# Kernel tuning notes

Measured on AMD Instinct MI355X. Metric: run time of the kernel, lower is better.

## Reference

```python
import jax, jax.numpy as jnp
import numpy as np

NEG_SLOPE = 0.2


def _gat_layer(x, edge_index, W, a_src, a_dst, b):
    """PyG GATConv: linear -> per-edge attention logits -> segment softmax over
    destination -> scatter-add weighted messages. Self-loops added (PyG default)."""
    N = x.shape[0]
    heads, out = a_src.shape
    loops = jnp.arange(N, dtype=edge_index.dtype)
    src = jnp.concatenate([edge_index[0], loops])
    dst = jnp.concatenate([edge_index[1], loops])
    xh = (x @ W).reshape(N, heads, out)                      # [N,H,D]
    alpha_s = (xh * a_src).sum(-1)                           # [N,H]
    alpha_d = (xh * a_dst).sum(-1)                           # [N,H]
    e = jax.nn.leaky_relu(alpha_s[src] + alpha_d[dst], NEG_SLOPE)  # [E,H]
    emax = jax.ops.segment_max(e, dst, num_segments=N)       # [N,H]
    ex = jnp.exp(e - emax[dst])
    den = jax.ops.segment_sum(ex, dst, num_segments=N)
    att = ex / (den[dst] + 1e-16)                            # [E,H]
    msg = xh[src] * att[..., None]                           # [E,H,D]
    o = jax.ops.segment_sum(msg, dst, num_segments=N)        # [N,H,D]
    return o.reshape(N, heads * out) + b


def _single_source_gnn(h, edge_index, params):
    n_layers = len(params)
    for i, (W, a_s, a_d, b) in enumerate(params):
        h = _gat_layer(h, edge_index, W, a_s, a_d, b)
        if i < n_layers - 1:
            h = jax.nn.relu(h)
    return h


def setup_inputs() -> dict:
    key = jax.random.key(0)
    B, N, H, heads, deg = 4, 2000, 64, 4, 32
    E = N * deg
    ks = jax.random.split(key, 20)

    def mk_edge_index(k):
        e = jax.random.randint(k, (2, B, E), 0, N)
        off = (jnp.arange(B) * N)[None, :, None]
        return (e + off).reshape(2, B * E).astype(jnp.int32)

    inp = {
        "h0_flat": jax.random.normal(ks[0], (B * N, H), jnp.float32),
        "edge_index_s1": mk_edge_index(ks[1]),
        "edge_index_s2": mk_edge_index(ks[2]),
    }
    dims = [(H, H * heads), (H * heads, H * heads)]
    i = 3
    for s in ("s1", "s2"):
        for l, (din, dout) in enumerate(dims):
            inp[f"W_{s}_{l}"] = jax.random.normal(ks[i], (din, dout), jnp.float32) * 0.1; i += 1
            inp[f"a_src_{s}_{l}"] = jax.random.normal(ks[i], (heads, H), jnp.float32) * 0.1; i += 1
            inp[f"a_dst_{s}_{l}"] = jax.random.normal(ks[i], (heads, H), jnp.float32) * 0.1; i += 1
            inp[f"b_{s}_{l}"] = jnp.zeros((dout,), jnp.float32)
    inp["batch_size"] = B
    inp["num_stocks"] = N
    return inp


def reference(h0_flat, edge_index_s1, edge_index_s2,
              W_s1_0, a_src_s1_0, a_dst_s1_0, b_s1_0,
              W_s1_1, a_src_s1_1, a_dst_s1_1, b_s1_1,
              W_s2_0, a_src_s2_0, a_dst_s2_0, b_s2_0,
              W_s2_1, a_src_s2_1, a_dst_s2_1, b_s2_1,
              batch_size, num_stocks):
    p1 = [(W_s1_0, a_src_s1_0, a_dst_s1_0, b_s1_0),
          (W_s1_1, a_src_s1_1, a_dst_s1_1, b_s1_1)]
    p2 = [(W_s2_0, a_src_s2_0, a_dst_s2_0, b_s2_0),
          (W_s2_1, a_src_s2_1, a_dst_s2_1, b_s2_1)]
    h1 = _single_source_gnn(h0_flat, edge_index_s1, p1)
    h2 = _single_source_gnn(h0_flat, edge_index_s2, p2)
    # dict of per-source outputs in torch -> stacked [n_sources, B*N, H*heads]
    return jnp.stack([h1, h2])
```

## Files before the change

### kernel.cpp

```cpp
#include <hip/hip_runtime.h>
#include <hip/hip_fp16.h>


#define NEG_SLOPE 0.2f
#define ELLW 96
#define EPT 8
#define NB_PREP 512

typedef _Float16 half8 __attribute__((ext_vector_type(8)));
typedef float floatx4 __attribute__((ext_vector_type(4)));

struct Args {
    const float* h0;
    const int *ei1, *ei2;
    const float *W10, *W11, *W20, *W21;
    const float *as10, *ad10, *b10, *as11, *ad11, *b11;
    const float *as20, *ad20, *b20, *as21, *ad21, *b21;
    _Float16 *Wt10, *Wt20, *Wt11, *Wt21;
    _Float16 *h0h;
    int *cnt, *slots;
    _Float16 *agg1, *agg2;
    _Float16 *xh1, *xh2;
    float *alS1, *alD1, *alS2, *alD2;
    float *out0, *out1;
    int N, E1, E2, AB;
};


__global__ __launch_bounds__(256) void mega_prep_kernel(Args a) {
    int b = blockIdx.x;
    int tid = threadIdx.x;

    if (b < NB_PREP) {
        int flat = b * 256 + tid;
        int GT = NB_PREP * 256;
        int totA = 32768;
        int totB = totA + 131072;
        int totC = totB + a.N * 64;
        for (int i = flat; i < totC; i += GT) {
            if (i < totA) {
                int s = i >> 14, rem = i & 16383;
                int c = rem >> 6, k = rem & 63;
                const float* W = s ? a.W20 : a.W10;
                _Float16* Wt = s ? a.Wt20 : a.Wt10;
                Wt[c * 64 + k] = (_Float16)W[k * 256 + c];
            } else if (i < totB) {
                int i2 = i - totA;
                int s = i2 >> 16, rem = i2 & 65535;
                int c = rem >> 8, k = rem & 255;
                const float* W = s ? a.W21 : a.W11;
                _Float16* Wt = s ? a.Wt21 : a.Wt11;
                Wt[c * 256 + k] = (_Float16)W[k * 256 + c];
            } else {
                int i3 = i - totB;
                a.h0h[i3] = (_Float16)a.h0[i3];
            }
        }
    } else if (b < NB_PREP + a.AB) {
        __shared__ float va[8][64];
        __shared__ float h0s[64][64];
        int ab = b - NB_PREP;
        int g0 = ab * 64;
        int s = (g0 >= a.N) ? 1 : 0;
        int i0 = g0 - s * a.N;
        const float* W0 = s ? a.W20 : a.W10;
        const float* aS = s ? a.as20 : a.as10;
        const float* aD = s ? a.ad20 : a.ad10;
        float* alS = s ? a.alS2 : a.alS1;
        float* alD = s ? a.alD2 : a.alD1;
#pragma unroll
        for (int o = 0; o < 2; o++) {
            int out = o * 256 + tid;
            int sel = out >> 8, rem = out & 255;
            int h = rem >> 6, t = rem & 63;
            const float* av = sel ? aD : aS;
            float acc = 0.f;
            const float* wrow = W0 + (size_t)t * 256 + h * 64;
            const float* arow = av + h * 64;
            for (int cc = 0; cc < 64; cc++) acc += wrow[cc] * arow[cc];
            va[sel * 4 + h][t] = acc;
        }
#pragma unroll
        for (int e = 0; e < 16; e++) {
            int idx = e * 256 + tid;
            h0s[idx >> 6][idx & 63] = a.h0[(size_t)(i0 + (idx >> 6)) * 64 + (idx & 63)];
        }
        __syncthreads();
        int r = tid >> 2, h = tid & 3;
        float sv = 0.f, dv = 0.f;
        for (int k = 0; k < 64; k++) {
            float x = h0s[r][k];
            sv += x * va[h][k];
            dv += x * va[4 + h][k];
        }
        alS[(i0 + r) * 4 + h] = sv;
        alD[(i0 + r) * 4 + h] = dv;
    } else {
        int sb = b - NB_PREP - a.AB;
        int rr = sb & 7;
        int chunk = sb >> 3;
        int cpx = (2 * a.N) >> 3;
        int glo = rr * cpx, ghi = glo + cpx;
        int tot1 = a.E1 + a.N;
        int tot = tot1 + a.E2 + a.N;
        int base = chunk * (256 * EPT);
#pragma unroll
        for (int k = 0; k < EPT; k++) {
            int j = base + k * 256 + tid;
            if (j >= tot) break;
            int s, jj; const int* ei; int E;
            if (j < tot1) { s = 0; jj = j;        ei = a.ei1; E = a.E1; }
            else          { s = 1; jj = j - tot1; ei = a.ei2; E = a.E2; }
            int dst = (jj < E) ? ei[E + jj] : (jj - E);
            int gg = s * a.N + dst;
            if (gg < glo || gg >= ghi) continue;
            int src = (jj < E) ? ei[jj] : dst;
            int pos = atomicAdd(&a.cnt[gg], 1);
            if (pos < ELLW) a.slots[(size_t)gg * ELLW + pos] = src;
        }
    }
}


__global__ __launch_bounds__(256) void attn_agg_kernel(Args a) {
    __shared__ float2 pairs[4][8][10];
    int tid = threadIdx.x;
    int h = tid >> 6, L = tid & 63, st = L >> 3, lc = L & 7;
    int b = blockIdx.x;
    int cpx = (2 * a.N) >> 3;
    int g = (b & 7) * cpx + (b >> 3);
    int s = (g >= a.N) ? 1 : 0;
    int dst = g - s * a.N;
    const float* alS = s ? a.alS2 : a.alS1;
    const float* alD = s ? a.alD2 : a.alD1;
    _Float16*    agg = s ? a.agg2 : a.agg1;

    const int* slots = a.slots + (size_t)g * ELLW;
    int pre = slots[L];
    int nd = a.cnt[g];
    if (nd > ELLW) nd = ELLW;
    float ad = alD[dst * 4 + h];
    const char* xb = (const char*)a.h0h + lc * 16;

    float acc[8] = {};
    float pden = 0.f;

    for (int c = 0; c < nd; c += 64) {
        int n = nd - c; if (n > 64) n = 64;
        int off = 0; float p = 0.f;
        if (L < n) {
            int src = (c == 0) ? pre : slots[c + L];
            float t = alS[src * 4 + h] + ad;
            t = (t > 0.f) ? t : NEG_SLOPE * t;
            p = __expf(t);
            off = src * 128;
        }
        pden += p;
        pairs[h][L & 7][L >> 3] = make_float2(__int_as_float(off), p);
        int iters = (n + 7) >> 3;
        for (int ii = 0; ii < iters; ii += 4) {
            float4 twoA = *(const float4*)&pairs[h][st][ii];
            float4 twoB = *(const float4*)&pairs[h][st][ii + 2];
            int   o0 = __float_as_int(twoA.x); float w0 = twoA.y;
            int   o1i = __float_as_int(twoA.z); float w1 = twoA.w;
            int   o2i = __float_as_int(twoB.x); float w2 = twoB.y;
            int   o3i = __float_as_int(twoB.z); float w3 = twoB.w;
            float4 r0 = *(const float4*)(xb + o0);
            float4 r1 = *(const float4*)(xb + o1i);
            float4 r2 = *(const float4*)(xb + o2i);
            float4 r3 = *(const float4*)(xb + o3i);
            const __half2* q0 = (const __half2*)&r0;
            const __half2* q1 = (const __half2*)&r1;
            const __half2* q2 = (const __half2*)&r2;
            const __half2* q3 = (const __half2*)&r3;
#pragma unroll
            for (int k = 0; k < 4; k++) {
                acc[2 * k + 0] += (float)q0[k].x * w0;
                acc[2 * k + 1] += (float)q0[k].y * w0;
                acc[2 * k + 0] += (float)q1[k].x * w1;
                acc[2 * k + 1] += (float)q1[k].y * w1;
                acc[2 * k + 0] += (float)q2[k].x * w2;
                acc[2 * k + 1] += (float)q2[k].y * w2;
                acc[2 * k + 0] += (float)q3[k].x * w3;
                acc[2 * k + 1] += (float)q3[k].y * w3;
            }
        }
    }
#pragma unroll
    for (int k = 0; k < 8; k++) {
        acc[k] += __shfl_xor(acc[k], 8);
        acc[k] += __shfl_xor(acc[k], 16);
        acc[k] += __shfl_xor(acc[k], 32);
    }
#pragma unroll
    for (int o2_ = 32; o2_ >= 1; o2_ >>= 1) pden += __shfl_xor(pden, o2_);

    if (st == 0) {
        float d = 1.0f / (pden + 1e-16f);
        int col = h * 64 + lc * 8;
        half8 ov;
#pragma unroll
        for (int k = 0; k < 8; k++) ov[k] = (_Float16)(acc[k] * d);
        *(half8*)(agg + (size_t)dst * 256 + col) = ov;
    }
}


__global__ __launch_bounds__(256) void fusedgemm_kernel(Args a) {
    __shared__ _Float16 hT[32][264];
    int half_ = (a.N / 32);
    int b = blockIdx.x;
    int s = (b >= half_);
    int bx = b - s * half_;
    int row0 = bx * 32;

    const _Float16* agg = s ? a.agg2 : a.agg1;
    const _Float16* Wt0 = s ? a.Wt20 : a.Wt10;
    const _Float16* Wt1 = s ? a.Wt21 : a.Wt11;
    const float* bias0  = s ? a.b20  : a.b10;
    const float* a_s    = s ? a.as21 : a.as11;
    const float* a_d    = s ? a.ad21 : a.ad11;
    _Float16* xh = s ? a.xh2 : a.xh1;
    float* alS = s ? a.alS2 : a.alS1;
    float* alD = s ? a.alD2 : a.alD1;

    int tid  = threadIdx.x;
    int wave = tid >> 6;
    int lane = tid & 63;
    int lo = lane & 15, hi = lane >> 4;
    int c0 = wave * 64;

    {
        floatx4 acc[2][4] = {};
#pragma unroll
        for (int ks = 0; ks < 2; ks++) {
            half8 af[2], bf[4];
#pragma unroll
            for (int f = 0; f < 2; f++)
                af[f] = *(const half8*)(agg + (size_t)(row0 + f * 16 + lo) * 256
                                        + c0 + ks * 32 + hi * 8);
#pragma unroll
            for (int cf = 0; cf < 4; cf++)
                bf[cf] = *(const half8*)(Wt0 + (size_t)(c0 + cf * 16 + lo) * 64
                                         + ks * 32 + hi * 8);
#pragma unroll
            for (int f = 0; f < 2; f++)
#pragma unroll
                for (int cf = 0; cf < 4; cf++)
                    acc[f][cf] = __builtin_amdgcn_mfma_f32_16x16x32_f16(
                        af[f], bf[cf], acc[f][cf], 0, 0, 0);
        }
        float bb[4];
#pragma unroll
        for (int cf = 0; cf < 4; cf++) bb[cf] = bias0[c0 + cf * 16 + lo];
#pragma unroll
        for (int f = 0; f < 2; f++)
#pragma unroll
            for (int cf = 0; cf < 4; cf++)
#pragma unroll
                for (int r = 0; r < 4; r++) {
                    int row = f * 16 + hi * 4 + r;
                    float v = acc[f][cf][r] + bb[cf];
                    hT[row][c0 + cf * 16 + lo] = (_Float16)fmaxf(v, 0.f);
                }
    }
    __syncthreads();

    floatx4 acc[2][4] = {};
#pragma unroll
    for (int ks = 0; ks < 8; ks++) {
        half8 af[2], bf[4];
#pragma unroll
        for (int f = 0; f < 2; f++)
            af[f] = *(const half8*)&hT[f * 16 + lo][ks * 32 + hi * 8];
#pragma unroll
        for (int cf = 0; cf < 4; cf++)
            bf[cf] = *(const half8*)(Wt1 + (size_t)(c0 + cf * 16 + lo) * 256
                                     + ks * 32 + hi * 8);
#pragma unroll
        for (int f = 0; f < 2; f++)
#pragma unroll
            for (int cf = 0; cf < 4; cf++)
                acc[f][cf] = __builtin_amdgcn_mfma_f32_16x16x32_f16(
                    af[f], bf[cf], acc[f][cf], 0, 0, 0);
    }

    float asw[4], adw[4];
#pragma unroll
    for (int cf = 0; cf < 4; cf++) {
        asw[cf] = a_s[c0 + cf * 16 + lo];
        adw[cf] = a_d[c0 + cf * 16 + lo];
    }
#pragma unroll
    for (int f = 0; f < 2; f++) {
#pragma unroll
        for (int r = 0; r < 4; r++) {
            int row = row0 + f * 16 + hi * 4 + r;
            float v0 = acc[f][0][r], v1 = acc[f][1][r];
            float v2 = acc[f][2][r], v3 = acc[f][3][r];
            _Float16* xrow = &xh[(size_t)row * 256 + c0 + lo];
            xrow[0]  = (_Float16)v0;
            xrow[16] = (_Float16)v1;
            xrow[32] = (_Float16)v2;
            xrow[48] = (_Float16)v3;
            float s1 = v0 * asw[0] + v1 * asw[1] + v2 * asw[2] + v3 * asw[3];
            float s2 = v0 * adw[0] + v1 * adw[1] + v2 * adw[2] + v3 * adw[3];
#pragma unroll
            for (int off = 1; off < 16; off <<= 1) {
                s1 += __shfl_xor(s1, off);
                s2 += __shfl_xor(s2, off);
            }
            if (lo == 0) {
                alS[row * 4 + wave] = s1;
                alD[row * 4 + wave] = s2;
            }
        }
    }
}


__global__ __launch_bounds__(256) void attn1_kernel(Args a) {
    __shared__ float2 pairs[4][8][10];
    int tid = threadIdx.x;
    int h = tid >> 6, L = tid & 63, st = L >> 3, lc = L & 7;
    int b = blockIdx.x;
    int cpx = (2 * a.N) >> 3;
    int g = (b & 7) * cpx + (b >> 3);
    int s = (g >= a.N) ? 1 : 0;
    int dst = g - s * a.N;
    const _Float16* xh = s ? a.xh2  : a.xh1;
    const float* alS   = s ? a.alS2 : a.alS1;
    const float* alD   = s ? a.alD2 : a.alD1;
    const float* bias  = s ? a.b21  : a.b11;
    float* out         = s ? a.out1 : a.out0;

    const int* slots = a.slots + (size_t)g * ELLW;
    int pre = slots[L];
    int nd = a.cnt[g];
    if (nd > ELLW) nd = ELLW;
    float ad = alD[dst * 4 + h];
    const char* xb = (const char*)xh + h * 128 + lc * 16;

    float acc[8] = {};
    float pden = 0.f;

    for (int c = 0; c < nd; c += 64) {
        int n = nd - c; if (n > 64) n = 64;
        int off = 0; float p = 0.f;
        if (L < n) {
            int src = (c == 0) ? pre : slots[c + L];
            float t = alS[src * 4 + h] + ad;
            t = (t > 0.f) ? t : NEG_SLOPE * t;
            p = __expf(t);
            off = src * 512;
        }
        pden += p;
        pairs[h][L & 7][L >> 3] = make_float2(__int_as_float(off), p);
        int iters = (n + 7) >> 3;
        for (int ii = 0; ii < iters; ii += 4) {
            float4 twoA = *(const float4*)&pairs[h][st][ii];
            float4 twoB = *(const float4*)&pairs[h][st][ii + 2];
            int   o0 = __float_as_int(twoA.x); float w0 = twoA.y;
            int   o1i = __float_as_int(twoA.z); float w1 = twoA.w;
            int   o2i = __float_as_int(twoB.x); float w2 = twoB.y;
            int   o3i = __float_as_int(twoB.z); float w3 = twoB.w;
            float4 r0 = *(const float4*)(xb + o0);
            float4 r1 = *(const float4*)(xb + o1i);
            float4 r2 = *(const float4*)(xb + o2i);
            float4 r3 = *(const float4*)(xb + o3i);
            const __half2* q0 = (const __half2*)&r0;
            const __half2* q1 = (const __half2*)&r1;
            const __half2* q2 = (const __half2*)&r2;
            const __half2* q3 = (const __half2*)&r3;
#pragma unroll
            for (int k = 0; k < 4; k++) {
                acc[2 * k + 0] += (float)q0[k].x * w0;
                acc[2 * k + 1] += (float)q0[k].y * w0;
                acc[2 * k + 0] += (float)q1[k].x * w1;
                acc[2 * k + 1] += (float)q1[k].y * w1;
                acc[2 * k + 0] += (float)q2[k].x * w2;
                acc[2 * k + 1] += (float)q2[k].y * w2;
                acc[2 * k + 0] += (float)q3[k].x * w3;
                acc[2 * k + 1] += (float)q3[k].y * w3;
            }
        }
    }
#pragma unroll
    for (int k = 0; k < 8; k++) {
        acc[k] += __shfl_xor(acc[k], 8);
        acc[k] += __shfl_xor(acc[k], 16);
        acc[k] += __shfl_xor(acc[k], 32);
    }
#pragma unroll
    for (int o2_ = 32; o2_ >= 1; o2_ >>= 1) pden += __shfl_xor(pden, o2_);

    if (st == 0) {
        float d = 1.0f / (pden + 1e-16f);
        int col = h * 64 + lc * 8;
        float4 bA = *(const float4*)&bias[col];
        float4 bB = *(const float4*)&bias[col + 4];
        float4 oA, oB;
        oA.x = acc[0] * d + bA.x; oA.y = acc[1] * d + bA.y;
        oA.z = acc[2] * d + bA.z; oA.w = acc[3] * d + bA.w;
        oB.x = acc[4] * d + bB.x; oB.y = acc[5] * d + bB.y;
        oB.z = acc[6] * d + bB.z; oB.w = acc[7] * d + bB.w;
        *(float4*)&out[(size_t)dst * 256 + col] = oA;
        *(float4*)&out[(size_t)dst * 256 + col + 4] = oB;
    }
}


extern "C" void kernel_launch(void* const* d_in, const int* in_sizes, int n_in,
                              void* d_out, int out_size, void* d_ws, size_t ws_size,
                              hipStream_t stream) {
    const int N  = in_sizes[0] / 64;
    const int E1 = in_sizes[1] / 2;
    const int E2 = in_sizes[2] / 2;

    char* base = (char*)d_ws;
    size_t off = 0;
    auto carve = [&](size_t bytes) -> void* {
        void* p = base + off;
        off += (bytes + 255) & ~(size_t)255;
        return p;
    };
    int* cnt        = (int*)carve((size_t)2 * N * 4);
    int* slots      = (int*)carve((size_t)2 * N * ELLW * 4);
    _Float16* agg1  = (_Float16*)carve((size_t)N * 256 * 2);
    _Float16* agg2  = (_Float16*)carve((size_t)N * 256 * 2);
    _Float16* xh1   = (_Float16*)carve((size_t)N * 256 * 2);
    _Float16* xh2   = (_Float16*)carve((size_t)N * 256 * 2);
    float* alS1     = (float*)carve((size_t)N * 4 * 4);
    float* alD1     = (float*)carve((size_t)N * 4 * 4);
    float* alS2     = (float*)carve((size_t)N * 4 * 4);
    float* alD2     = (float*)carve((size_t)N * 4 * 4);
    _Float16* Wt10  = (_Float16*)carve((size_t)256 * 64 * 2);
    _Float16* Wt20  = (_Float16*)carve((size_t)256 * 64 * 2);
    _Float16* Wt11  = (_Float16*)carve((size_t)256 * 256 * 2);
    _Float16* Wt21  = (_Float16*)carve((size_t)256 * 256 * 2);
    _Float16* h0h   = (_Float16*)carve((size_t)N * 64 * 2);
    (void)ws_size; (void)n_in;

    Args a;
    a.h0 = (const float*)d_in[0];
    a.ei1 = (const int*)d_in[1];
    a.ei2 = (const int*)d_in[2];
    a.W10 = (const float*)d_in[3];  a.as10 = (const float*)d_in[4];
    a.ad10 = (const float*)d_in[5]; a.b10 = (const float*)d_in[6];
    a.W11 = (const float*)d_in[7];  a.as11 = (const float*)d_in[8];
    a.ad11 = (const float*)d_in[9]; a.b11 = (const float*)d_in[10];
    a.W20 = (const float*)d_in[11]; a.as20 = (const float*)d_in[12];
    a.ad20 = (const float*)d_in[13]; a.b20 = (const float*)d_in[14];
    a.W21 = (const float*)d_in[15]; a.as21 = (const float*)d_in[16];
    a.ad21 = (const float*)d_in[17]; a.b21 = (const float*)d_in[18];
    a.Wt10 = Wt10; a.Wt20 = Wt20; a.Wt11 = Wt11; a.Wt21 = Wt21;
    a.h0h = h0h;
    a.cnt = cnt; a.slots = slots;
    a.agg1 = agg1; a.agg2 = agg2;
    a.xh1 = xh1; a.xh2 = xh2;
    a.alS1 = alS1; a.alD1 = alD1; a.alS2 = alS2; a.alD2 = alD2;
    a.out0 = (float*)d_out; a.out1 = (float*)d_out + (size_t)N * 256;
    a.N = N; a.E1 = E1; a.E2 = E2;
    a.AB = (2 * N) / 64;

    int tot = (E1 + N) + (E2 + N);
    int chunks = (tot + 256 * EPT - 1) / (256 * EPT);
    int scatterBlocks = chunks * 8;

    hipMemsetAsync(cnt, 0, (size_t)2 * N * 4, stream);
    mega_prep_kernel<<<NB_PREP + a.AB + scatterBlocks, 256, 0, stream>>>(a);
    attn_agg_kernel<<<2 * N, 256, 0, stream>>>(a);
    fusedgemm_kernel<<<(N / 32) * 2, 256, 0, stream>>>(a);
    attn1_kernel<<<2 * N, 256, 0, stream>>>(a);
}
```

Baseline: 110.6 us.

## Stagger per-source stages so GEMM blocks share kernels with attention blocks

```diff
diff --git a/kernel.cpp b/kernel.cpp
--- a/kernel.cpp
+++ b/kernel.cpp
@@ -23,7 +23,12 @@
     _Float16 *xh1, *xh2;
     float *alS1, *alD1, *alS2, *alD2;
     float *out0, *out1;
-    int N, E1, E2, AB;
+    int N, E1, E2, AB, GB;
+};
+
+union SM {
+    _Float16 hT[16][264];
+    float2 pairs[4][8][10];
 };
 
 
@@ -122,15 +127,10 @@
 }
 
 
-__global__ __launch_bounds__(256) void attn_agg_kernel(Args a) {
-    __shared__ float2 pairs[4][8][10];
+__device__ __forceinline__ void attn_agg_node(const Args& a, int s, int dst, SM& sm) {
     int tid = threadIdx.x;
     int h = tid >> 6, L = tid & 63, st = L >> 3, lc = L & 7;
-    int b = blockIdx.x;
-    int cpx = (2 * a.N) >> 3;
-    int g = (b & 7) * cpx + (b >> 3);
-    int s = (g >= a.N) ? 1 : 0;
-    int dst = g - s * a.N;
+    int g = s * a.N + dst;
     const float* alS = s ? a.alS2 : a.alS1;
     const float* alD = s ? a.alD2 : a.alD1;
     _Float16*    agg = s ? a.agg2 : a.agg1;
@@ -156,11 +156,11 @@
             off = src * 128;
         }
         pden += p;
-        pairs[h][L & 7][L >> 3] = make_float2(__int_as_float(off), p);
+        sm.pairs[h][L & 7][L >> 3] = make_float2(__int_as_float(off), p);
         int iters = (n + 7) >> 3;
         for (int ii = 0; ii < iters; ii += 4) {
-            float4 twoA = *(const float4*)&pairs[h][st][ii];
-            float4 twoB = *(const float4*)&pairs[h][st][ii + 2];
+            float4 twoA = *(const float4*)&sm.pairs[h][st][ii];
+            float4 twoB = *(const float4*)&sm.pairs[h][st][ii + 2];
             int   o0 = __float_as_int(twoA.x); float w0 = twoA.y;
             int   o1i = __float_as_int(twoA.z); float w1 = twoA.w;
             int   o2i = __float_as_int(twoB.x); float w2 = twoB.y;
@@ -206,128 +206,10 @@
 }
 
 
-__global__ __launch_bounds__(256) void fusedgemm_kernel(Args a) {
-    __shared__ _Float16 hT[32][264];
-    int half_ = (a.N / 32);
-    int b = blockIdx.x;
-    int s = (b >= half_);
-    int bx = b - s * half_;
-    int row0 = bx * 32;
-
-    const _Float16* agg = s ? a.agg2 : a.agg1;
-    const _Float16* Wt0 = s ? a.Wt20 : a.Wt10;
-    const _Float16* Wt1 = s ? a.Wt21 : a.Wt11;
-    const float* bias0  = s ? a.b20  : a.b10;
-    const float* a_s    = s ? a.as21 : a.as11;
-    const float* a_d    = s ? a.ad21 : a.ad11;
-    _Float16* xh = s ? a.xh2 : a.xh1;
-    float* alS = s ? a.alS2 : a.alS1;
-    float* alD = s ? a.alD2 : a.alD1;
-
-    int tid  = threadIdx.x;
-    int wave = tid >> 6;
-    int lane = tid & 63;
-    int lo = lane & 15, hi = lane >> 4;
-    int c0 = wave * 64;
-
-    {
-        floatx4 acc[2][4] = {};
-#pragma unroll
-        for (int ks = 0; ks < 2; ks++) {
-            half8 af[2], bf[4];
-#pragma unroll
-            for (int f = 0; f < 2; f++)
-                af[f] = *(const half8*)(agg + (size_t)(row0 + f * 16 + lo) * 256
-                                        + c0 + ks * 32 + hi * 8);
-#pragma unroll
-            for (int cf = 0; cf < 4; cf++)
-                bf[cf] = *(const half8*)(Wt0 + (size_t)(c0 + cf * 16 + lo) * 64
-                                         + ks * 32 + hi * 8);
-#pragma unroll
-            for (int f = 0; f < 2; f++)
-#pragma unroll
-                for (int cf = 0; cf < 4; cf++)
-                    acc[f][cf] = __builtin_amdgcn_mfma_f32_16x16x32_f16(
-                        af[f], bf[cf], acc[f][cf], 0, 0, 0);
-        }
-        float bb[4];
-#pragma unroll
-        for (int cf = 0; cf < 4; cf++) bb[cf] = bias0[c0 + cf * 16 + lo];
-#pragma unroll
-        for (int f = 0; f < 2; f++)
-#pragma unroll
-            for (int cf = 0; cf < 4; cf++)
-#pragma unroll
-                for (int r = 0; r < 4; r++) {
-                    int row = f * 16 + hi * 4 + r;
-                    float v = acc[f][cf][r] + bb[cf];
-                    hT[row][c0 + cf * 16 + lo] = (_Float16)fmaxf(v, 0.f);
-                }
-    }
-    __syncthreads();
-
-    floatx4 acc[2][4] = {};
-#pragma unroll
-    for (int ks = 0; ks < 8; ks++) {
-        half8 af[2], bf[4];
-#pragma unroll
-        for (int f = 0; f < 2; f++)
-            af[f] = *(const half8*)&hT[f * 16 + lo][ks * 32 + hi * 8];
-#pragma unroll
-        for (int cf = 0; cf < 4; cf++)
-            bf[cf] = *(const half8*)(Wt1 + (size_t)(c0 + cf * 16 + lo) * 256
-                                     + ks * 32 + hi * 8);
-#pragma unroll
-        for (int f = 0; f < 2; f++)
-#pragma unroll
-            for (int cf = 0; cf < 4; cf++)
-                acc[f][cf] = __builtin_amdgcn_mfma_f32_16x16x32_f16(
-                    af[f], bf[cf], acc[f][cf], 0, 0, 0);
-    }
-
-    float asw[4], adw[4];
-#pragma unroll
-    for (int cf = 0; cf < 4; cf++) {
-        asw[cf] = a_s[c0 + cf * 16 + lo];
-        adw[cf] = a_d[c0 + cf * 16 + lo];
-    }
-#pragma unroll
-    for (int f = 0; f < 2; f++) {
-#pragma unroll
-        for (int r = 0; r < 4; r++) {
-            int row = row0 + f * 16 + hi * 4 + r;
-            float v0 = acc[f][0][r], v1 = acc[f][1][r];
-            float v2 = acc[f][2][r], v3 = acc[f][3][r];
-            _Float16* xrow = &xh[(size_t)row * 256 + c0 + lo];
-            xrow[0]  = (_Float16)v0;
-            xrow[16] = (_Float16)v1;
-            xrow[32] = (_Float16)v2;
-            xrow[48] = (_Float16)v3;
-            float s1 = v0 * asw[0] + v1 * asw[1] + v2 * asw[2] + v3 * asw[3];
-            float s2 = v0 * adw[0] + v1 * adw[1] + v2 * adw[2] + v3 * adw[3];
-#pragma unroll
-            for (int off = 1; off < 16; off <<= 1) {
-                s1 += __shfl_xor(s1, off);
-                s2 += __shfl_xor(s2, off);
-            }
-            if (lo == 0) {
-                alS[row * 4 + wave] = s1;
-                alD[row * 4 + wave] = s2;
-            }
-        }
-    }
-}
-
-
-__global__ __launch_bounds__(256) void attn1_kernel(Args a) {
-    __shared__ float2 pairs[4][8][10];
+__device__ __forceinline__ void attn1_node(const Args& a, int s, int dst, SM& sm) {
     int tid = threadIdx.x;
     int h = tid >> 6, L = tid & 63, st = L >> 3, lc = L & 7;
-    int b = blockIdx.x;
-    int cpx = (2 * a.N) >> 3;
-    int g = (b & 7) * cpx + (b >> 3);
-    int s = (g >= a.N) ? 1 : 0;
-    int dst = g - s * a.N;
+    int g = s * a.N + dst;
     const _Float16* xh = s ? a.xh2  : a.xh1;
     const float* alS   = s ? a.alS2 : a.alS1;
     const float* alD   = s ? a.alD2 : a.alD1;
@@ -355,11 +237,11 @@
             off = src * 512;
         }
         pden += p;
-        pairs[h][L & 7][L >> 3] = make_float2(__int_as_float(off), p);
+        sm.pairs[h][L & 7][L >> 3] = make_float2(__int_as_float(off), p);
         int iters = (n + 7) >> 3;
         for (int ii = 0; ii < iters; ii += 4) {
-            float4 twoA = *(const float4*)&pairs[h][st][ii];
-            float4 twoB = *(const float4*)&pairs[h][st][ii + 2];
+            float4 twoA = *(const float4*)&sm.pairs[h][st][ii];
+            float4 twoB = *(const float4*)&sm.pairs[h][st][ii + 2];
             int   o0 = __float_as_int(twoA.x); float w0 = twoA.y;
             int   o1i = __float_as_int(twoA.z); float w1 = twoA.w;
             int   o2i = __float_as_int(twoB.x); float w2 = twoB.y;
@@ -407,6 +289,141 @@
         *(float4*)&out[(size_t)dst * 256 + col] = oA;
         *(float4*)&out[(size_t)dst * 256 + col + 4] = oB;
     }
+}
+
+
+__device__ __forceinline__ void fused16(const Args& a, int s, int row0, SM& sm) {
+    const _Float16* agg = s ? a.agg2 : a.agg1;
+    const _Float16* Wt0 = s ? a.Wt20 : a.Wt10;
+    const _Float16* Wt1 = s ? a.Wt21 : a.Wt11;
+    const float* bias0  = s ? a.b20  : a.b10;
+    const float* a_s    = s ? a.as21 : a.as11;
+    const float* a_d    = s ? a.ad21 : a.ad11;
+    _Float16* xh = s ? a.xh2 : a.xh1;
+    float* alS = s ? a.alS2 : a.alS1;
+    float* alD = s ? a.alD2 : a.alD1;
+
+    int tid  = threadIdx.x;
+    int wave = tid >> 6;
+    int lane = tid & 63;
+    int lo = lane & 15, hi = lane >> 4;
+    int c0 = wave * 64;
+
+    {
+        floatx4 acc[4] = {};
+#pragma unroll
+        for (int ks = 0; ks < 2; ks++) {
+            half8 af = *(const half8*)(agg + (size_t)(row0 + lo) * 256
+                                       + c0 + ks * 32 + hi * 8);
+            half8 bf[4];
+#pragma unroll
+            for (int cf = 0; cf < 4; cf++)
+                bf[cf] = *(const half8*)(Wt0 + (size_t)(c0 + cf * 16 + lo) * 64
+                                         + ks * 32 + hi * 8);
+#pragma unroll
+            for (int cf = 0; cf < 4; cf++)
+                acc[cf] = __builtin_amdgcn_mfma_f32_16x16x32_f16(
+                    af, bf[cf], acc[cf], 0, 0, 0);
+        }
+        float bb[4];
+#pragma unroll
+        for (int cf = 0; cf < 4; cf++) bb[cf] = bias0[c0 + cf * 16 + lo];
+#pragma unroll
+        for (int cf = 0; cf < 4; cf++)
+#pragma unroll
+            for (int r = 0; r < 4; r++) {
+                int row = hi * 4 + r;
+                float v = acc[cf][r] + bb[cf];
+                sm.hT[row][c0 + cf * 16 + lo] = (_Float16)fmaxf(v, 0.f);
+            }
+    }
+    __syncthreads();
+
+    floatx4 acc[4] = {};
+#pragma unroll
+    for (int ks = 0; ks < 8; ks++) {
+        half8 af = *(const half8*)&sm.hT[lo][ks * 32 + hi * 8];
+        half8 bf[4];
+#pragma unroll
+        for (int cf = 0; cf < 4; cf++)
+            bf[cf] = *(const half8*)(Wt1 + (size_t)(c0 + cf * 16 + lo) * 256
+                                     + ks * 32 + hi * 8);
+#pragma unroll
+        for (int cf = 0; cf < 4; cf++)
+            acc[cf] = __builtin_amdgcn_mfma_f32_16x16x32_f16(
+                af, bf[cf], acc[cf], 0, 0, 0);
+    }
+
+    float asw[4], adw[4];
+#pragma unroll
+    for (int cf = 0; cf < 4; cf++) {
+        asw[cf] = a_s[c0 + cf * 16 + lo];
+        adw[cf] = a_d[c0 + cf * 16 + lo];
+    }
+#pragma unroll
+    for (int r = 0; r < 4; r++) {
+        int row = row0 + hi * 4 + r;
+        float v0 = acc[0][r], v1 = acc[1][r], v2 = acc[2][r], v3 = acc[3][r];
+        _Float16* xrow = &xh[(size_t)row * 256 + c0 + lo];
+        xrow[0]  = (_Float16)v0;
+        xrow[16] = (_Float16)v1;
+        xrow[32] = (_Float16)v2;
+        xrow[48] = (_Float16)v3;
+        float s1 = v0 * asw[0] + v1 * asw[1] + v2 * asw[2] + v3 * asw[3];
+        float s2 = v0 * adw[0] + v1 * adw[1] + v2 * adw[2] + v3 * adw[3];
+#pragma unroll
+        for (int off = 1; off < 16; off <<= 1) {
+            s1 += __shfl_xor(s1, off);
+            s2 += __shfl_xor(s2, off);
+        }
+        if (lo == 0) {
+            alS[row * 4 + wave] = s1;
+            alD[row * 4 + wave] = s2;
+        }
+    }
+}
+
+
+__global__ __launch_bounds__(256) void attn_agg0_kernel(Args a) {
+    __shared__ SM sm;
+    int b = blockIdx.x;
+    int cpx = a.N >> 3;
+    int dst = (b & 7) * cpx + (b >> 3);
+    attn_agg_node(a, 0, dst, sm);
+}
+
+__global__ __launch_bounds__(256) void mix1_kernel(Args a) {
+    __shared__ SM sm;
+    int b = blockIdx.x;
+    if (b < a.GB) {
+        fused16(a, 0, b * 16, sm);
+    } else {
+        int bb = b - a.GB;
+        int cpx = a.N >> 3;
+        int dst = (bb & 7) * cpx + (bb >> 3);
+        attn_agg_node(a, 1, dst, sm);
+    }
+}
+
+__global__ __launch_bounds__(256) void mix2_kernel(Args a) {
+    __shared__ SM sm;
+    int b = blockIdx.x;
+    if (b < a.GB) {
+        fused16(a, 1, b * 16, sm);
+    } else {
+        int bb = b - a.GB;
+        int cpx = a.N >> 3;
+        int dst = (bb & 7) * cpx + (bb >> 3);
+        attn1_node(a, 0, dst, sm);
+    }
+}
+
+__global__ __launch_bounds__(256) void attn1b_kernel(Args a) {
+    __shared__ SM sm;
+    int b = blockIdx.x;
+    int cpx = a.N >> 3;
+    int dst = (b & 7) * cpx + (b >> 3);
+    attn1_node(a, 1, dst, sm);
 }
 
 
@@ -462,6 +479,7 @@
     a.out0 = (float*)d_out; a.out1 = (float*)d_out + (size_t)N * 256;
     a.N = N; a.E1 = E1; a.E2 = E2;
     a.AB = (2 * N) / 64;
+    a.GB = N / 16;
 
     int tot = (E1 + N) + (E2 + N);
     int chunks = (tot + 256 * EPT - 1) / (256 * EPT);
@@ -469,7 +487,8 @@
 
     hipMemsetAsync(cnt, 0, (size_t)2 * N * 4, stream);
     mega_prep_kernel<<<NB_PREP + a.AB + scatterBlocks, 256, 0, stream>>>(a);
-    attn_agg_kernel<<<2 * N, 256, 0, stream>>>(a);
-    fusedgemm_kernel<<<(N / 32) * 2, 256, 0, stream>>>(a);
-    attn1_kernel<<<2 * N, 256, 0, stream>>>(a);
-}
+    attn_agg0_kernel<<<N, 256, 0, stream>>>(a);
+    mix1_kernel<<<a.GB + N, 256, 0, stream>>>(a);
+    mix2_kernel<<<a.GB + N, 256, 0, stream>>>(a);
+    attn1b_kernel<<<N, 256, 0, stream>>>(a);
+}
```

Result: slower. 123.5 us (+11.7%).
